# Optimization experiments

Measured on AMD Instinct MI355X. Metric: run time of the kernel, lower is better.

Reference implementation:

```python
import jax, jax.numpy as jnp
import numpy as np

DIM = 1536
NHEADS = 12
HDIM = DIM // NHEADS  # 128
EPS = 1e-6
LOCAL_ATTN_SIZE = 3
SINK_SIZE = 1
MAX_ATTN = 32760 if LOCAL_ATTN_SIZE == -1 else LOCAL_ATTN_SIZE * 1560  # 4680


def _rms(x, g):
    # WanRMSNorm over last dim
    return x * jax.lax.rsqrt(jnp.mean(x * x, axis=-1, keepdims=True) + EPS) * g


def _rope(x, f, h, w, fr, fi, start_frame):
    # x: [b, s, n, d] with s == f*h*w; fr/fi: [1024, d//2] real/imag of complex rotations
    b, s, n, d = x.shape
    c = d // 2
    c0 = c - 2 * (c // 3)
    c1 = c // 3
    fc = jax.lax.complex(fr, fi)  # [1024, c]
    xr = x.reshape(b, s, n, c, 2)
    xc = jax.lax.complex(xr[..., 0], xr[..., 1])  # [b, s, n, c]
    ff = fc[start_frame:start_frame + f, :c0]      # [f, c0]
    fh = fc[:h, c0:c0 + c1]                        # [h, c1]
    fw = fc[:w, c0 + c1:c0 + 2 * c1]               # [w, c1]
    freqs_i = jnp.concatenate([
        jnp.broadcast_to(ff[:, None, None, :], (f, h, w, c0)),
        jnp.broadcast_to(fh[None, :, None, :], (f, h, w, c1)),
        jnp.broadcast_to(fw[None, None, :, :], (f, h, w, c1)),
    ], axis=-1).reshape(1, s, 1, c)
    y = xc * freqs_i
    return jnp.stack([y.real, y.imag], axis=-1).reshape(b, s, n, d)


def _attn(q, k, v):
    # plain SDPA (decode path of the module uses no mask on the gathered window)
    scale = 1.0 / np.sqrt(q.shape[-1]).astype(np.float32)
    logits = jnp.einsum('bqnd,bknd->bnqk', q, k) * scale
    p = jax.nn.softmax(logits, axis=-1)
    return jnp.einsum('bnqk,bknd->bqnd', p, v)


def _forward(x, cache_k, cache_v, freqs_real, freqs_imag,
             wq, bq, wk, bk, wv, bv, wo, bo, gq, gk,
             f_frames, height, width, current_start, global_end_index, local_end_index):
    b, s, _ = x.shape
    n, d = NHEADS, HDIM
    frame_seqlen = height * width
    start_frame = current_start // frame_seqlen

    q = _rms(x @ wq + bq, gq).reshape(b, s, n, d)
    k = _rms(x @ wk + bk, gk).reshape(b, s, n, d)
    v = (x @ wv + bv).reshape(b, s, n, d)

    rq = _rope(q, f_frames, height, width, freqs_real, freqs_imag, start_frame)
    rk = _rope(k, f_frames, height, width, freqs_real, freqs_imag, start_frame)

    current_end = current_start + s
    sink_tokens = SINK_SIZE * frame_seqlen
    kv_size = cache_k.shape[1]
    is_recompute = (current_end <= global_end_index) and (current_start > 0)

    kc, vc = cache_k, cache_v
    if LOCAL_ATTN_SIZE != -1 and current_end > global_end_index and s + local_end_index > kv_size:
        # evict oldest non-sink tokens, roll the rest toward the sink region
        num_evicted = s + local_end_index - kv_size
        num_rolled = local_end_index - num_evicted - sink_tokens
        src = slice(sink_tokens + num_evicted, sink_tokens + num_evicted + num_rolled)
        kc = kc.at[:, sink_tokens:sink_tokens + num_rolled].set(jax.lax.stop_gradient(cache_k[:, src]))
        vc = vc.at[:, sink_tokens:sink_tokens + num_rolled].set(jax.lax.stop_gradient(cache_v[:, src]))
        new_local_end = local_end_index + current_end - global_end_index - num_evicted
    else:
        new_local_end = local_end_index + current_end - global_end_index
    local_start = new_local_end - s
    write_start = max(local_start, sink_tokens) if is_recompute else local_start
    off = max(0, write_start - local_start)
    wl = max(0, new_local_end - write_start)
    if wl > 0:
        kc = kc.at[:, write_start:new_local_end].set(rk[:, off:off + wl])
        vc = vc.at[:, write_start:new_local_end].set(v[:, off:off + wl])

    if sink_tokens > 0:
        budget = MAX_ATTN - sink_tokens
        if budget > 0:
            lo = max(sink_tokens, new_local_end - budget)
            kcat = jnp.concatenate([kc[:, :sink_tokens], kc[:, lo:new_local_end]], axis=1)
            vcat = jnp.concatenate([vc[:, :sink_tokens], vc[:, lo:new_local_end]], axis=1)
        else:
            kcat, vcat = kc[:, :sink_tokens], vc[:, :sink_tokens]
        o = _attn(rq, kcat, vcat)
    else:
        ws = max(0, new_local_end - MAX_ATTN)
        o = _attn(rq, kc[:, ws:new_local_end], vc[:, ws:new_local_end])

    return o.reshape(b, s, DIM) @ wo + bo


def setup_inputs() -> dict:
    key = jax.random.key(0)
    ks = jax.random.split(key, 12)
    B, S, CACHE = 1, 1560, 4680
    sc = 0.02
    # RoPE tables as unit-magnitude complex rotations
    ang = jax.random.uniform(ks[0], (1024, HDIM // 2), jnp.float32, 0.0, 2.0 * np.pi)
    return {
        'x': jax.random.normal(ks[1], (B, S, DIM), jnp.float32),
        'cache_k': jax.random.normal(ks[2], (B, CACHE, NHEADS, HDIM), jnp.float32),
        'cache_v': jax.random.normal(ks[3], (B, CACHE, NHEADS, HDIM), jnp.float32),
        'freqs_real': jnp.cos(ang),
        'freqs_imag': jnp.sin(ang),
        'wq': jax.random.normal(ks[4], (DIM, DIM), jnp.float32) * sc,
        'bq': jnp.zeros((DIM,), jnp.float32),
        'wk': jax.random.normal(ks[5], (DIM, DIM), jnp.float32) * sc,
        'bk': jnp.zeros((DIM,), jnp.float32),
        'wv': jax.random.normal(ks[6], (DIM, DIM), jnp.float32) * sc,
        'bv': jnp.zeros((DIM,), jnp.float32),
        'wo': jax.random.normal(ks[7], (DIM, DIM), jnp.float32) * sc,
        'bo': jnp.zeros((DIM,), jnp.float32),
        'gq': jnp.ones((DIM,), jnp.float32),
        'gk': jnp.ones((DIM,), jnp.float32),
        'f_frames': 1,
        'height': 30,
        'width': 52,
        'current_start': 4680,
        'global_end_index': 4680,
        'local_end_index': 4680,
    }


def reference(x, cache_k, cache_v, freqs_real, freqs_imag,
              wq, bq, wk, bk, wv, bv, wo, bo, gq, gk,
              f_frames, height, width, current_start, global_end_index, local_end_index):
    return _forward(x, cache_k, cache_v, freqs_real, freqs_imag,
                    wq, bq, wk, bk, wv, bv, wo, bo, gq, gk,
                    f_frames, height, width, current_start, global_end_index, local_end_index)
```

## Files before the change

### kernel.cpp

```cpp
#include <hip/hip_runtime.h>
#include <cstdint>
#include <cstddef>

typedef unsigned int  u32;
typedef unsigned short u16;
typedef short s16x8 __attribute__((ext_vector_type(8)));
typedef float f32x4 __attribute__((ext_vector_type(4)));

#define DIM     1536
#define NH      12
#define HD      128
#define SEQ     1560
#define MPAD    1664
#define NKV     4680
#define NKPAD   4736
#define ROLL0   3120
#define NQK     4608
#define START_FRAME 3
#define NEGINF  -3.0e4f
#define NSPLIT  4
#define SPLITKC 1216

__device__ __forceinline__ u16 f2bf(float f){
  u32 u = __builtin_bit_cast(u32, f);
  u32 r = (u + 0x7fffu + ((u >> 16) & 1u)) >> 16;
  return (u16)r;
}

__global__ void k_pre(const float* __restrict__ x, u16* __restrict__ xp,
                      u16* __restrict__ Kc, u16* __restrict__ VT,
                      u16* __restrict__ Qr, u16* __restrict__ Opad,
                      float* __restrict__ sumsq,
                      const float* __restrict__ ck, const float* __restrict__ cv){
  __shared__ u32 tile[64][65];
  int b = blockIdx.x, t = threadIdx.x;
  if (b < 244){
    int i = b * 256 + t;
    uint4 z = make_uint4(0u, 0u, 0u, 0u);
    if (i < 10752){
      int h = i / 896, r = i % 896;
      ((uint4*)(Kc + ((size_t)h * NKPAD + NKV) * 128))[r] = z;
    } else if (i < 21504){
      int j = i - 10752; int row = j / 7, c = j % 7;
      ((uint4*)(VT + (size_t)row * NKPAD + NKV))[c] = z;
    } else if (i < 41472){
      int j = i - 21504; int h = j / 1664, r = j % 1664;
      ((uint4*)(Qr + ((size_t)h * MPAD + SEQ) * 128))[r] = z;
    } else if (i < 61440){
      int r = i - 41472;
      ((uint4*)(Opad + (size_t)SEQ * DIM))[r] = z;
    } else if (i < 62272){
      ((uint4*)sumsq)[i - 61440] = z;
    }
  } else if (b < 1492){
    int i = (b - 244) * 256 + t;
    const int n_src = SEQ * DIM / 8;
    u16 o[8] = {0,0,0,0,0,0,0,0};
    if (i < n_src){
      float4 a = ((const float4*)x)[2*i];
      float4 c = ((const float4*)x)[2*i + 1];
      o[0]=f2bf(a.x); o[1]=f2bf(a.y); o[2]=f2bf(a.z); o[3]=f2bf(a.w);
      o[4]=f2bf(c.x); o[5]=f2bf(c.y); o[6]=f2bf(c.z); o[7]=f2bf(c.w);
    }
    uint4 v = make_uint4((u32)o[0]|((u32)o[1]<<16), (u32)o[2]|((u32)o[3]<<16),
                         (u32)o[4]|((u32)o[5]<<16), (u32)o[6]|((u32)o[7]<<16));
    ((uint4*)xp)[i] = v;
  } else if (b < 3832){
    int i = (b - 1492) * 256 + t;
    int p = i / 192, j = i - p * 192;
    int src = (p < SEQ) ? p : p + SEQ;
    int h = j >> 4, d = (j & 15) * 8;
    const float* s = ck + (size_t)src * DIM + j * 8;
    float4 a = ((const float4*)s)[0], bb = ((const float4*)s)[1];
    uint4 v = make_uint4((u32)f2bf(a.x)|((u32)f2bf(a.y)<<16), (u32)f2bf(a.z)|((u32)f2bf(a.w)<<16),
                         (u32)f2bf(bb.x)|((u32)f2bf(bb.y)<<16), (u32)f2bf(bb.z)|((u32)f2bf(bb.w)<<16));
    *(uint4*)(Kc + (size_t)(h * NKPAD + p) * 128 + d) = v;
  } else {
    int idx = b - 3832;
    int p0 = (idx % 49) * 64, hd0 = (idx / 49) * 64;
    int pr = t >> 4, cg = t & 15;
#pragma unroll
    for (int i = 0; i < 4; i++){
      int p = p0 + pr + i * 16;
      if (p < ROLL0){
        int src = (p < SEQ) ? p : p + SEQ;
        float4 v = *(const float4*)(cv + (size_t)src * DIM + hd0 + cg * 4);
        tile[pr + i*16][cg*4+0] = f2bf(v.x); tile[pr + i*16][cg*4+1] = f2bf(v.y);
        tile[pr + i*16][cg*4+2] = f2bf(v.z); tile[pr + i*16][cg*4+3] = f2bf(v.w);
      }
    }
    __syncthreads();
    int hd = t >> 2, pg = t & 3;
    int pbase = p0 + pg * 16;
    if (pbase < ROLL0){
      u32 wds[8];
#pragma unroll
      for (int j = 0; j < 8; j++)
        wds[j] = (tile[pg*16 + 2*j][hd] & 0xffffu) | (tile[pg*16 + 2*j + 1][hd] << 16);
      u16* q = VT + (size_t)(hd0 + hd) * NKPAD + pbase;
      *(uint4*)q       = make_uint4(wds[0], wds[1], wds[2], wds[3]);
      *(uint4*)(q + 8) = make_uint4(wds[4], wds[5], wds[6], wds[7]);
    }
  }
}

__global__ void k_transpose_w(const float* __restrict__ wq, const float* __restrict__ wk,
                              const float* __restrict__ wv, const float* __restrict__ wo,
                              u16* __restrict__ WTqkv, u16* __restrict__ WTo){
  __shared__ u32 tile[64][65];
  int z = blockIdx.z;
  const float* w = (z==0)?wq:(z==1)?wk:(z==2)?wv:wo;
  u16* dst = (z < 3) ? (WTqkv + (size_t)z * DIM * DIM) : WTo;
  int r0 = blockIdx.x * 64, c0 = blockIdx.y * 64;
  int t = threadIdx.x;
  int rr = t >> 4, cg = t & 15;
#pragma unroll
  for (int i = 0; i < 4; i++){
    int r = rr + i * 16;
    float4 v = *(const float4*)(w + (size_t)(r0 + r) * DIM + c0 + cg * 4);
    tile[r][cg*4+0] = f2bf(v.x); tile[r][cg*4+1] = f2bf(v.y);
    tile[r][cg*4+2] = f2bf(v.z); tile[r][cg*4+3] = f2bf(v.w);
  }
  __syncthreads();
  int c = t >> 2, rg = t & 3;
  u32 wds[8];
#pragma unroll
  for (int j = 0; j < 8; j++)
    wds[j] = (tile[rg*16 + 2*j][c] & 0xffffu) | (tile[rg*16 + 2*j + 1][c] << 16);
  u16* q = dst + (size_t)(c0 + c) * DIM + r0 + rg * 16;
  *(uint4*)q       = make_uint4(wds[0], wds[1], wds[2], wds[3]);
  *(uint4*)(q + 8) = make_uint4(wds[4], wds[5], wds[6], wds[7]);
}

#define LDK 40
__global__ __launch_bounds__(256) void k_gemm_qkv(
    const u16* __restrict__ A, const u16* __restrict__ B,
    const float* __restrict__ biasq, const float* __restrict__ biask, const float* __restrict__ biasv,
    float* __restrict__ Y, float* __restrict__ sumsq, u16* __restrict__ VT){
  __shared__ u16 As[128*LDK];
  __shared__ u16 Bs[128*LDK];
  int m0 = blockIdx.y * 128, n0 = blockIdx.x * 128;
  int t = threadIdx.x, w = t >> 6, lane = t & 63, quad = lane >> 4, lc = lane & 15;
  int wm = w & 1, wn = w >> 1;
  int sr = t >> 1, sh = (t & 1) * 16;
  f32x4 acc[4][4] = {};
  uint4 pa0, pa1, pb0, pb1;
  {
    const uint4* ga = (const uint4*)(A + (size_t)(m0 + sr) * DIM + sh);
    const uint4* gb = (const uint4*)(B + (size_t)(n0 + sr) * DIM + sh);
    pa0 = ga[0]; pa1 = ga[1]; pb0 = gb[0]; pb1 = gb[1];
  }
  for (int kt = 0; kt < DIM/32; kt++){
    __syncthreads();
    *(uint4*)(As + sr * LDK + sh)     = pa0;
    *(uint4*)(As + sr * LDK + sh + 8) = pa1;
    *(uint4*)(Bs + sr * LDK + sh)     = pb0;
    *(uint4*)(Bs + sr * LDK + sh + 8) = pb1;
    __syncthreads();
    if (kt + 1 < DIM/32){
      int k0 = (kt + 1) * 32;
      const uint4* ga = (const uint4*)(A + (size_t)(m0 + sr) * DIM + k0 + sh);
      const uint4* gb = (const uint4*)(B + (size_t)(n0 + sr) * DIM + k0 + sh);
      pa0 = ga[0]; pa1 = ga[1]; pb0 = gb[0]; pb1 = gb[1];
    }
    s16x8 af[4], bf[4];
#pragma unroll
    for (int mt = 0; mt < 4; mt++) af[mt] = *(const s16x8*)(As + (wm*64 + mt*16 + lc) * LDK + quad * 8);
#pragma unroll
    for (int nt = 0; nt < 4; nt++) bf[nt] = *(const s16x8*)(Bs + (wn*64 + nt*16 + lc) * LDK + quad * 8);
#pragma unroll
    for (int mt = 0; mt < 4; mt++)
#pragma unroll
      for (int nt = 0; nt < 4; nt++)
        acc[mt][nt] = __builtin_amdgcn_mfma_f32_16x16x32_bf16(af[mt], bf[nt], acc[mt][nt], 0, 0, 0);
  }
  const float* bias; int cbase; int which;
  if (n0 < DIM)        { bias = biasq; cbase = 0;     which = 0; }
  else if (n0 < 2*DIM) { bias = biask; cbase = DIM;   which = 1; }
  else                 { bias = biasv; cbase = 2*DIM; which = 2; }
  float bvals[4];
#pragma unroll
  for (int nt = 0; nt < 4; nt++) bvals[nt] = bias[n0 - cbase + wn*64 + nt*16 + lc];
  if (which == 2){
#pragma unroll
    for (int mt = 0; mt < 4; mt++){
      int row0 = m0 + wm*64 + mt*16 + quad*4;
      if (row0 < SEQ){
#pragma unroll
        for (int nt = 0; nt < 4; nt++){
          int hd = (n0 - 2*DIM) + wn*64 + nt*16 + lc;
          u32 lo = (u32)f2bf(acc[mt][nt][0] + bvals[nt]) | ((u32)f2bf(acc[mt][nt][1] + bvals[nt]) << 16);
          u32 hi = (u32)f2bf(acc[mt][nt][2] + bvals[nt]) | ((u32)f2bf(acc[mt][nt][3] + bvals[nt]) << 16);
          *(uint2*)(VT + (size_t)hd * NKPAD + ROLL0 + row0) = make_uint2(lo, hi);
        }
      }
    }
  } else {
#pragma unroll
    for (int mt = 0; mt < 4; mt++){
      int row0 = m0 + wm*64 + mt*16 + quad*4;
      float ss[4] = {0.f, 0.f, 0.f, 0.f};
#pragma unroll
      for (int nt = 0; nt < 4; nt++){
        int col = n0 + wn*64 + nt*16 + lc;
#pragma unroll
        for (int r = 0; r < 4; r++){
          float y = acc[mt][nt][r] + bvals[nt];
          Y[(size_t)(row0 + r) * NQK + col] = y;
          ss[r] += y * y;
        }
      }
      float* dst = sumsq + (which ? MPAD : 0);
#pragma unroll
      for (int r = 0; r < 4; r++){
        float v = ss[r];
        v += __shfl_xor(v, 1); v += __shfl_xor(v, 2); v += __shfl_xor(v, 4); v += __shfl_xor(v, 8);
        if (lc == 0) atomicAdd(&dst[row0 + r], v);
      }
    }
  }
}

__global__ void k_rope_qk(const float* __restrict__ Y, const float* __restrict__ sumsq,
                          const float* __restrict__ gq, const float* __restrict__ gk,
                          const float* __restrict__ fre, const float* __restrict__ fim,
                          u16* __restrict__ Qr, u16* __restrict__ Kc){
  int pos = blockIdx.x;
  int t = threadIdx.x;
  float scq = rsqrtf(sumsq[pos]        * (1.0f/1536.0f) + 1e-6f);
  float sck = rsqrtf(sumsq[MPAD + pos] * (1.0f/1536.0f) + 1e-6f);
  int hrow = pos / 52, wrow = pos % 52;
#pragma unroll
  for (int i = 0; i < 3; i++){
    int p = t + i * 256;
    int head = p >> 6, j = p & 63;
    int frow = (j < 22) ? START_FRAME : ((j < 43) ? hrow : wrow);
    float cr = fre[frow * 64 + j], ci = fim[frow * 64 + j];
    int d0 = head * 128 + 2 * j;
    float2 yq = *(const float2*)(Y + (size_t)pos * NQK + d0);
    float qa = yq.x * scq * gq[d0];
    float qb = yq.y * scq * gq[d0 + 1];
    u32 oq = (u32)f2bf(qa * cr - qb * ci) | ((u32)f2bf(qa * ci + qb * cr) << 16);
    *(u32*)(Qr + (size_t)(head * MPAD + pos) * 128 + 2 * j) = oq;
    float2 yk = *(const float2*)(Y + (size_t)pos * NQK + DIM + d0);
    float ka = yk.x * sck * gk[d0];
    float kb = yk.y * sck * gk[d0 + 1];
    u32 ok = (u32)f2bf(ka * cr - kb * ci) | ((u32)f2bf(ka * ci + kb * cr) << 16);
    *(u32*)(Kc + (size_t)(head * NKPAD + ROLL0 + pos) * 128 + 2 * j) = ok;
  }
}

#define DEFER_THR 8.0f
__global__ __launch_bounds__(512, 4) void k_attn(const u16* __restrict__ Qr, const u16* __restrict__ Kc,
                                                 const u16* __restrict__ VT,
                                                 float* __restrict__ Opart, float* __restrict__ ml){
  __shared__ u16 Ks[64 * 128];
  __shared__ u16 Vs[128 * 64];
  int h = blockIdx.y, qb = blockIdx.x, sp = blockIdx.z;
  int t = threadIdx.x, w = t >> 6, lane = t & 63, quad = lane >> 4, lc = lane & 15;
  int qbase = qb * 128 + w * 16;
  const u16* Qbase = Qr + (size_t)(h * MPAD + qbase + lc) * 128;
  s16x8 qf[4];
#pragma unroll
  for (int kk = 0; kk < 4; kk++) qf[kk] = *(const s16x8*)(Qbase + kk * 32 + quad * 8);
  f32x4 oacc[8] = {};
  float m_ = NEGINF;
  float l_ = 0.f;
  const float scale = 0.08838834764831845f;
  const u16* Kh = Kc + (size_t)h * NKPAD * 128;
  const u16* Vh = VT + (size_t)h * 128 * NKPAD;
  int kr0 = t >> 4,          kg0 = (t & 15) * 8;
  int kr1 = (t + 512) >> 4,  kg1 = ((t + 512) & 15) * 8;
  int vd0 = t >> 3,          vp0 = (t & 7) * 8;
  int vd1 = (t + 512) >> 3,  vp1 = ((t + 512) & 7) * 8;
  int ksw0 = kr0 * 128 + (kg0 ^ ((kr0 & 7) << 3));
  int ksw1 = kr1 * 128 + (kg1 ^ ((kr1 & 7) << 3));
  int vsw0 = vd0 * 64  + (vp0 ^ ((vd0 & 7) << 3));
  int vsw1 = vd1 * 64  + (vp1 ^ ((vd1 & 7) << 3));
  int xork = (lc & 7) << 3;
  int aa = (lc + ((quad & 1) << 5)) << 2;
  int ab = aa + 64;
  int hi = quad >> 1;

  int kc0 = sp * SPLITKC;
  int kc1 = (sp == NSPLIT-1) ? NKPAD : kc0 + SPLITKC;
  uint4 kp0, kp1, vq0, vq1;
  {
    int kc = kc0;
    kp0 = *(const uint4*)(Kh + (size_t)(kc + kr0) * 128 + kg0);
    kp1 = *(const uint4*)(Kh + (size_t)(kc + kr1) * 128 + kg1);
    vq0 = *(const uint4*)(Vh + (size_t)vd0 * NKPAD + kc + vp0);
    vq1 = *(const uint4*)(Vh + (size_t)vd1 * NKPAD + kc + vp1);
  }
  for (int kc = kc0; kc < kc1; kc += 64){
    __syncthreads();
    *(uint4*)(Ks + ksw0) = kp0;
    *(uint4*)(Ks + ksw1) = kp1;
    *(uint4*)(Vs + vsw0) = vq0;
    *(uint4*)(Vs + vsw1) = vq1;
    __syncthreads();
    if (kc + 64 < kc1){
      int kn = kc + 64;
      kp0 = *(const uint4*)(Kh + (size_t)(kn + kr0) * 128 + kg0);
      kp1 = *(const uint4*)(Kh + (size_t)(kn + kr1) * 128 + kg1);
      vq0 = *(const uint4*)(Vh + (size_t)vd0 * NKPAD + kn + vp0);
      vq1 = *(const uint4*)(Vh + (size_t)vd1 * NKPAD + kn + vp1);
    }
    float s[4][4];
    __builtin_amdgcn_s_setprio(1);
#pragma unroll
    for (int nt = 0; nt < 4; nt++){
      f32x4 acc = {};
      int p = nt * 16 + lc;
#pragma unroll
      for (int kk = 0; kk < 4; kk++){
        s16x8 kf = *(const s16x8*)(Ks + p * 128 + (((kk * 4 + quad) * 8) ^ xork));
        acc = __builtin_amdgcn_mfma_f32_16x16x32_bf16(kf, qf[kk], acc, 0, 0, 0);
      }
#pragma unroll
      for (int r = 0; r < 4; r++) s[nt][r] = acc[r] * scale;
    }
    __builtin_amdgcn_s_setprio(0);
    if (kc + 64 > NKV){
#pragma unroll
      for (int nt = 0; nt < 4; nt++){
        int keyb = kc + nt * 16 + quad * 4;
#pragma unroll
        for (int r = 0; r < 4; r++) if (keyb + r >= NKV) s[nt][r] = NEGINF;
      }
    }
    float mx = fmaxf(fmaxf(s[0][0], s[0][1]), fmaxf(s[0][2], s[0][3]));
#pragma unroll
    for (int nt = 1; nt < 4; nt++)
      mx = fmaxf(mx, fmaxf(fmaxf(s[nt][0], s[nt][1]), fmaxf(s[nt][2], s[nt][3])));
    mx = fmaxf(mx, __shfl_xor(mx, 16));
    mx = fmaxf(mx, __shfl_xor(mx, 32));
    if (__any(mx > m_ + DEFER_THR)){
      float mnew = fmaxf(m_, mx);
      float alpha = __expf(m_ - mnew);
      m_ = mnew; l_ *= alpha;
      float alr[4];
#pragma unroll
      for (int r = 0; r < 4; r++) alr[r] = __shfl(alpha, quad * 4 + r);
#pragma unroll
      for (int dt = 0; dt < 8; dt++){
        f32x4 oo = oacc[dt];
#pragma unroll
        for (int r = 0; r < 4; r++) oo[r] *= alr[r];
        oacc[dt] = oo;
      }
    }
#pragma unroll
    for (int nt = 0; nt < 4; nt++)
#pragma unroll
      for (int r = 0; r < 4; r++) s[nt][r] = __expf(s[nt][r] - m_);
    float sum = (s[0][0] + s[0][1]) + (s[0][2] + s[0][3]);
#pragma unroll
    for (int nt = 1; nt < 4; nt++)
      sum += (s[nt][0] + s[nt][1]) + (s[nt][2] + s[nt][3]);
    sum += __shfl_xor(sum, 16);
    sum += __shfl_xor(sum, 32);
    l_ += sum;
    u32 w01[4], w23[4];
#pragma unroll
    for (int nt = 0; nt < 4; nt++){
      w01[nt] = (u32)f2bf(s[nt][0]) | ((u32)f2bf(s[nt][1]) << 16);
      w23[nt] = (u32)f2bf(s[nt][2]) | ((u32)f2bf(s[nt][3]) << 16);
    }
    u32 x0, x1;
    uint4 A0, A1;
    x0 = (u32)__builtin_amdgcn_ds_bpermute(aa, (int)w01[0]);
    x1 = (u32)__builtin_amdgcn_ds_bpermute(aa, (int)w01[1]);
    A0.x = hi ? x1 : x0;
    x0 = (u32)__builtin_amdgcn_ds_bpermute(aa, (int)w23[0]);
    x1 = (u32)__builtin_amdgcn_ds_bpermute(aa, (int)w23[1]);
    A0.y = hi ? x1 : x0;
    x0 = (u32)__builtin_amdgcn_ds_bpermute(ab, (int)w01[0]);
    x1 = (u32)__builtin_amdgcn_ds_bpermute(ab, (int)w01[1]);
    A0.z = hi ? x1 : x0;
    x0 = (u32)__builtin_amdgcn_ds_bpermute(ab, (int)w23[0]);
    x1 = (u32)__builtin_amdgcn_ds_bpermute(ab, (int)w23[1]);
    A0.w = hi ? x1 : x0;
    x0 = (u32)__builtin_amdgcn_ds_bpermute(aa, (int)w01[2]);
    x1 = (u32)__builtin_amdgcn_ds_bpermute(aa, (int)w01[3]);
    A1.x = hi ? x1 : x0;
    x0 = (u32)__builtin_amdgcn_ds_bpermute(aa, (int)w23[2]);
    x1 = (u32)__builtin_amdgcn_ds_bpermute(aa, (int)w23[3]);
    A1.y = hi ? x1 : x0;
    x0 = (u32)__builtin_amdgcn_ds_bpermute(ab, (int)w01[2]);
    x1 = (u32)__builtin_amdgcn_ds_bpermute(ab, (int)w01[3]);
    A1.z = hi ? x1 : x0;
    x0 = (u32)__builtin_amdgcn_ds_bpermute(ab, (int)w23[2]);
    x1 = (u32)__builtin_amdgcn_ds_bpermute(ab, (int)w23[3]);
    A1.w = hi ? x1 : x0;
    s16x8 a0 = __builtin_bit_cast(s16x8, A0);
    s16x8 a1 = __builtin_bit_cast(s16x8, A1);
    __builtin_amdgcn_s_setprio(1);
#pragma unroll
    for (int dt = 0; dt < 8; dt++){
      int d = dt * 16 + lc;
      s16x8 v0 = *(const s16x8*)(Vs + d * 64 + ((quad * 8) ^ xork));
      s16x8 v1 = *(const s16x8*)(Vs + d * 64 + ((32 + quad * 8) ^ xork));
      oacc[dt] = __builtin_amdgcn_mfma_f32_16x16x32_bf16(a0, v0, oacc[dt], 0, 0, 0);
      oacc[dt] = __builtin_amdgcn_mfma_f32_16x16x32_bf16(a1, v1, oacc[dt], 0, 0, 0);
    }
    __builtin_amdgcn_s_setprio(0);
  }
  float mr[4], lr[4];
#pragma unroll
  for (int r = 0; r < 4; r++){
    mr[r] = __shfl(m_, quad * 4 + r);
    lr[r] = __shfl(l_, quad * 4 + r);
  }
  float* Ob = Opart + ((size_t)(sp * NH + h) * SEQ) * 128;
  float* mlb = ml + ((size_t)(sp * NH + h) * SEQ) * 2;
#pragma unroll
  for (int dt = 0; dt < 8; dt++)
#pragma unroll
    for (int r = 0; r < 4; r++){
      int row = qbase + quad * 4 + r;
      if (row < SEQ) Ob[(size_t)row * 128 + dt * 16 + lc] = oacc[dt][r];
    }
  if (lc == 0){
#pragma unroll
    for (int r = 0; r < 4; r++){
      int row = qbase + quad * 4 + r;
      if (row < SEQ){
        mlb[row * 2 + 0] = mr[r];
        mlb[row * 2 + 1] = lr[r];
      }
    }
  }
}

__global__ void k_attn_cmb(const float* __restrict__ Opart, const float* __restrict__ ml,
                           u16* __restrict__ Og){
  int row = blockIdx.x, h = blockIdx.y, d = threadIdx.x;
  float m[NSPLIT], l[NSPLIT];
  float M = NEGINF;
#pragma unroll
  for (int s = 0; s < NSPLIT; s++){
    m[s] = ml[((size_t)(s * NH + h) * SEQ + row) * 2 + 0];
    l[s] = ml[((size_t)(s * NH + h) * SEQ + row) * 2 + 1];
    M = fmaxf(M, m[s]);
  }
  float L = 0.f, o = 0.f;
#pragma unroll
  for (int s = 0; s < NSPLIT; s++){
    float wgt = __expf(m[s] - M);
    L += wgt * l[s];
    o += wgt * Opart[((size_t)(s * NH + h) * SEQ + row) * 128 + d];
  }
  Og[(size_t)row * DIM + h * 128 + d] = f2bf(o / L);
}

__global__ __launch_bounds__(256) void k_gemm_out(const u16* __restrict__ A, const u16* __restrict__ B,
                                                  const float* __restrict__ bo, float* __restrict__ out){
  __shared__ u16 As[128*LDK];
  __shared__ u16 Bs[128*LDK];
  int m0 = blockIdx.y * 128, n0 = blockIdx.x * 128;
  int t = threadIdx.x, w = t >> 6, lane = t & 63, quad = lane >> 4, lc = lane & 15;
  int wm = w & 1, wn = w >> 1;
  int sr = t >> 1, sh = (t & 1) * 16;
  f32x4 acc[4][4] = {};
  uint4 pa0, pa1, pb0, pb1;
  {
    const uint4* ga = (const uint4*)(A + (size_t)(m0 + sr) * DIM + sh);
    const uint4* gb = (const uint4*)(B + (size_t)(n0 + sr) * DIM + sh);
    pa0 = ga[0]; pa1 = ga[1]; pb0 = gb[0]; pb1 = gb[1];
  }
  for (int kt = 0; kt < DIM/32; kt++){
    __syncthreads();
    *(uint4*)(As + sr * LDK + sh)     = pa0;
    *(uint4*)(As + sr * LDK + sh + 8) = pa1;
    *(uint4*)(Bs + sr * LDK + sh)     = pb0;
    *(uint4*)(Bs + sr * LDK + sh + 8) = pb1;
    __syncthreads();
    if (kt + 1 < DIM/32){
      int k0 = (kt + 1) * 32;
      const uint4* ga = (const uint4*)(A + (size_t)(m0 + sr) * DIM + k0 + sh);
      const uint4* gb = (const uint4*)(B + (size_t)(n0 + sr) * DIM + k0 + sh);
      pa0 = ga[0]; pa1 = ga[1]; pb0 = gb[0]; pb1 = gb[1];
    }
    s16x8 af[4], bf[4];
#pragma unroll
    for (int mt = 0; mt < 4; mt++) af[mt] = *(const s16x8*)(As + (wm*64 + mt*16 + lc) * LDK + quad * 8);
#pragma unroll
    for (int nt = 0; nt < 4; nt++) bf[nt] = *(const s16x8*)(Bs + (wn*64 + nt*16 + lc) * LDK + quad * 8);
#pragma unroll
    for (int mt = 0; mt < 4; mt++)
#pragma unroll
      for (int nt = 0; nt < 4; nt++)
        acc[mt][nt] = __builtin_amdgcn_mfma_f32_16x16x32_bf16(af[mt], bf[nt], acc[mt][nt], 0, 0, 0);
  }
  float bvals[4];
#pragma unroll
  for (int nt = 0; nt < 4; nt++) bvals[nt] = bo[n0 + wn*64 + nt*16 + lc];
#pragma unroll
  for (int mt = 0; mt < 4; mt++){
    int row0 = m0 + wm*64 + mt*16 + quad*4;
#pragma unroll
    for (int nt = 0; nt < 4; nt++){
      int col = n0 + wn*64 + nt*16 + lc;
#pragma unroll
      for (int r = 0; r < 4; r++){
        int row = row0 + r;
        if (row < SEQ) out[(size_t)row * DIM + col] = acc[mt][nt][r] + bvals[nt];
      }
    }
  }
}

extern "C" void kernel_launch(void* const* d_in, const int* in_sizes, int n_in,
                              void* d_out, int out_size, void* d_ws, size_t ws_size,
                              hipStream_t stream){
  const float* x   = (const float*)d_in[0];
  const float* ck  = (const float*)d_in[1];
  const float* cv  = (const float*)d_in[2];
  const float* fre = (const float*)d_in[3];
  const float* fim = (const float*)d_in[4];
  const float* wq  = (const float*)d_in[5];
  const float* bq  = (const float*)d_in[6];
  const float* wk  = (const float*)d_in[7];
  const float* bk  = (const float*)d_in[8];
  const float* wv  = (const float*)d_in[9];
  const float* bv  = (const float*)d_in[10];
  const float* wo  = (const float*)d_in[11];
  const float* bo  = (const float*)d_in[12];
  const float* gq  = (const float*)d_in[13];
  const float* gk  = (const float*)d_in[14];

  char* ws = (char*)d_ws;
  size_t off = 0;
  u16*   xpad  = (u16*)(ws + off);  off += (size_t)MPAD * DIM * 2;
  u16*   WTqkv = (u16*)(ws + off);  off += (size_t)3 * DIM * DIM * 2;
  float* Y     = (float*)(ws + off); off += (size_t)MPAD * NQK * 4;
  u16*   WTo   = (u16*)(ws + off);  off += (size_t)DIM * DIM * 2;
  float* sumsq = (float*)(ws + off); off += (size_t)2 * MPAD * 4;
  u16*   Qr    = (u16*)(ws + off);  off += (size_t)NH * MPAD * 128 * 2;
  u16*   Kc    = (u16*)(ws + off);  off += (size_t)NH * NKPAD * 128 * 2;
  u16*   VT    = (u16*)(ws + off);  off += (size_t)NH * 128 * NKPAD * 2;
  u16*   Opad  = (u16*)(ws + off);  off += (size_t)MPAD * DIM * 2;
  if (off > ws_size) return;
  float* Opart = (float*)ws;
  float* ml    = (float*)(ws + (size_t)NSPLIT * NH * SEQ * 128 * 4);

  k_pre         <<<dim3(5008), 256, 0, stream>>>(x, xpad, Kc, VT, Qr, Opad, sumsq, ck, cv);
  k_transpose_w <<<dim3(24, 24, 4), 256, 0, stream>>>(wq, wk, wv, wo, WTqkv, WTo);
  k_gemm_qkv    <<<dim3(NQK/128, MPAD/128), 256, 0, stream>>>(xpad, WTqkv, bq, bk, bv, Y, sumsq, VT);
  k_rope_qk     <<<dim3(SEQ), 256, 0, stream>>>(Y, sumsq, gq, gk, fre, fim, Qr, Kc);
  k_attn        <<<dim3(MPAD/128, NH, NSPLIT), 512, 0, stream>>>(Qr, Kc, VT, Opart, ml);
  k_attn_cmb    <<<dim3(SEQ, NH), 128, 0, stream>>>(Opart, ml, Opad);
  k_gemm_out    <<<dim3(DIM/128, MPAD/128), 256, 0, stream>>>(Opad, WTo, bo, (float*)d_out);
}
```

Baseline: 357.4 us.

## Switch attention kernel to 32x32x16 MFMA with 32 query rows per wave

Rewrites the flash-attention inner loop to use 32x32x16 bf16 MFMA tiles, giving each wave 32 query rows instead of 16 and halving the block to 256 threads (4 waves). Each K/V tile loaded into shared memory is now reused by more rows per wave, the shuffle work for the softmax row max/sum shrinks, and the P-matrix lane exchange uses fewer bpermutes. In exchange, register pressure per thread rises (larger accumulators and Q fragments), occupancy hints change, and each thread must issue more global loads per tile.

Result: slower. 495.9 us (+38.8%).

```diff
diff --git a/kernel.cpp b/kernel.cpp
--- a/kernel.cpp
+++ b/kernel.cpp
@@ -6,6 +6,7 @@
 typedef unsigned short u16;
 typedef short s16x8 __attribute__((ext_vector_type(8)));
 typedef float f32x4 __attribute__((ext_vector_type(4)));
+typedef float f32x16 __attribute__((ext_vector_type(16)));
 
 #define DIM     1536
 #define NH      12
@@ -251,184 +252,166 @@
 }
 
 #define DEFER_THR 8.0f
-__global__ __launch_bounds__(512, 4) void k_attn(const u16* __restrict__ Qr, const u16* __restrict__ Kc,
+__global__ __launch_bounds__(256, 2) void k_attn(const u16* __restrict__ Qr, const u16* __restrict__ Kc,
                                                  const u16* __restrict__ VT,
                                                  float* __restrict__ Opart, float* __restrict__ ml){
   __shared__ u16 Ks[64 * 128];
   __shared__ u16 Vs[128 * 64];
   int h = blockIdx.y, qb = blockIdx.x, sp = blockIdx.z;
-  int t = threadIdx.x, w = t >> 6, lane = t & 63, quad = lane >> 4, lc = lane & 15;
-  int qbase = qb * 128 + w * 16;
-  const u16* Qbase = Qr + (size_t)(h * MPAD + qbase + lc) * 128;
-  s16x8 qf[4];
-#pragma unroll
-  for (int kk = 0; kk < 4; kk++) qf[kk] = *(const s16x8*)(Qbase + kk * 32 + quad * 8);
-  f32x4 oacc[8] = {};
-  float m_ = NEGINF;
-  float l_ = 0.f;
+  int t = threadIdx.x, w = t >> 6, lane = t & 63;
+  int l31 = lane & 31, hi = lane >> 5;
+  int qbase = qb * 128 + w * 32;
+  const u16* Qbase = Qr + (size_t)(h * MPAD + qbase + l31) * 128 + hi * 8;
+  s16x8 qf[8];
+#pragma unroll
+  for (int ds = 0; ds < 8; ds++) qf[ds] = *(const s16x8*)(Qbase + ds * 16);
+  f32x16 oacc[4] = {};
+  float m_ = NEGINF, l_ = 0.f;
   const float scale = 0.08838834764831845f;
   const u16* Kh = Kc + (size_t)h * NKPAD * 128;
   const u16* Vh = VT + (size_t)h * 128 * NKPAD;
-  int kr0 = t >> 4,          kg0 = (t & 15) * 8;
-  int kr1 = (t + 512) >> 4,  kg1 = ((t + 512) & 15) * 8;
-  int vd0 = t >> 3,          vp0 = (t & 7) * 8;
-  int vd1 = (t + 512) >> 3,  vp1 = ((t + 512) & 7) * 8;
-  int ksw0 = kr0 * 128 + (kg0 ^ ((kr0 & 7) << 3));
-  int ksw1 = kr1 * 128 + (kg1 ^ ((kr1 & 7) << 3));
-  int vsw0 = vd0 * 64  + (vp0 ^ ((vd0 & 7) << 3));
-  int vsw1 = vd1 * 64  + (vp1 ^ ((vd1 & 7) << 3));
-  int xork = (lc & 7) << 3;
-  int aa = (lc + ((quad & 1) << 5)) << 2;
-  int ab = aa + 64;
-  int hi = quad >> 1;
+  int kr[4], kg[4], ksw[4], vd[4], vp[4], vsw[4];
+#pragma unroll
+  for (int i = 0; i < 4; i++){
+    int n = t + i * 256;
+    kr[i] = n >> 4;  kg[i] = (n & 15) * 8;
+    ksw[i] = kr[i] * 128 + (kg[i] ^ ((kr[i] & 7) << 3));
+    vd[i] = n >> 3;  vp[i] = (n & 7) * 8;
+    vsw[i] = vd[i] * 64 + (vp[i] ^ ((vd[i] & 7) << 3));
+  }
+  int xork = (lane & 7) << 3;
+  int xaddr = (lane ^ 32) << 2;
 
   int kc0 = sp * SPLITKC;
   int kc1 = (sp == NSPLIT-1) ? NKPAD : kc0 + SPLITKC;
-  uint4 kp0, kp1, vq0, vq1;
-  {
-    int kc = kc0;
-    kp0 = *(const uint4*)(Kh + (size_t)(kc + kr0) * 128 + kg0);
-    kp1 = *(const uint4*)(Kh + (size_t)(kc + kr1) * 128 + kg1);
-    vq0 = *(const uint4*)(Vh + (size_t)vd0 * NKPAD + kc + vp0);
-    vq1 = *(const uint4*)(Vh + (size_t)vd1 * NKPAD + kc + vp1);
+  uint4 kp[4], vq[4];
+#pragma unroll
+  for (int i = 0; i < 4; i++){
+    kp[i] = *(const uint4*)(Kh + (size_t)(kc0 + kr[i]) * 128 + kg[i]);
+    vq[i] = *(const uint4*)(Vh + (size_t)vd[i] * NKPAD + kc0 + vp[i]);
   }
   for (int kc = kc0; kc < kc1; kc += 64){
     __syncthreads();
-    *(uint4*)(Ks + ksw0) = kp0;
-    *(uint4*)(Ks + ksw1) = kp1;
-    *(uint4*)(Vs + vsw0) = vq0;
-    *(uint4*)(Vs + vsw1) = vq1;
+#pragma unroll
+    for (int i = 0; i < 4; i++){
+      *(uint4*)(Ks + ksw[i]) = kp[i];
+      *(uint4*)(Vs + vsw[i]) = vq[i];
+    }
     __syncthreads();
     if (kc + 64 < kc1){
       int kn = kc + 64;
-      kp0 = *(const uint4*)(Kh + (size_t)(kn + kr0) * 128 + kg0);
-      kp1 = *(const uint4*)(Kh + (size_t)(kn + kr1) * 128 + kg1);
-      vq0 = *(const uint4*)(Vh + (size_t)vd0 * NKPAD + kn + vp0);
-      vq1 = *(const uint4*)(Vh + (size_t)vd1 * NKPAD + kn + vp1);
-    }
-    float s[4][4];
+#pragma unroll
+      for (int i = 0; i < 4; i++){
+        kp[i] = *(const uint4*)(Kh + (size_t)(kn + kr[i]) * 128 + kg[i]);
+        vq[i] = *(const uint4*)(Vh + (size_t)vd[i] * NKPAD + kn + vp[i]);
+      }
+    }
+    f32x16 sac[2];
     __builtin_amdgcn_s_setprio(1);
 #pragma unroll
-    for (int nt = 0; nt < 4; nt++){
-      f32x4 acc = {};
-      int p = nt * 16 + lc;
-#pragma unroll
-      for (int kk = 0; kk < 4; kk++){
-        s16x8 kf = *(const s16x8*)(Ks + p * 128 + (((kk * 4 + quad) * 8) ^ xork));
-        acc = __builtin_amdgcn_mfma_f32_16x16x32_bf16(kf, qf[kk], acc, 0, 0, 0);
-      }
-#pragma unroll
-      for (int r = 0; r < 4; r++) s[nt][r] = acc[r] * scale;
+    for (int kt = 0; kt < 2; kt++){
+      f32x16 acc = {};
+      const u16* kb = Ks + (kt * 32 + l31) * 128;
+#pragma unroll
+      for (int ds = 0; ds < 8; ds++){
+        s16x8 kf = *(const s16x8*)(kb + (((ds * 2 + hi) * 8) ^ xork));
+        acc = __builtin_amdgcn_mfma_f32_32x32x16_bf16(kf, qf[ds], acc, 0, 0, 0);
+      }
+      sac[kt] = acc;
     }
     __builtin_amdgcn_s_setprio(0);
+#pragma unroll
+    for (int kt = 0; kt < 2; kt++)
+#pragma unroll
+      for (int r = 0; r < 16; r++) sac[kt][r] *= scale;
     if (kc + 64 > NKV){
 #pragma unroll
-      for (int nt = 0; nt < 4; nt++){
-        int keyb = kc + nt * 16 + quad * 4;
-#pragma unroll
-        for (int r = 0; r < 4; r++) if (keyb + r >= NKV) s[nt][r] = NEGINF;
-      }
-    }
-    float mx = fmaxf(fmaxf(s[0][0], s[0][1]), fmaxf(s[0][2], s[0][3]));
-#pragma unroll
-    for (int nt = 1; nt < 4; nt++)
-      mx = fmaxf(mx, fmaxf(fmaxf(s[nt][0], s[nt][1]), fmaxf(s[nt][2], s[nt][3])));
-    mx = fmaxf(mx, __shfl_xor(mx, 16));
+      for (int kt = 0; kt < 2; kt++)
+#pragma unroll
+        for (int r = 0; r < 16; r++){
+          int key = kc + kt * 32 + (r & 3) + 8 * (r >> 2) + 4 * hi;
+          if (key >= NKV) sac[kt][r] = NEGINF;
+        }
+    }
+    float mx = sac[0][0];
+#pragma unroll
+    for (int r = 1; r < 16; r++) mx = fmaxf(mx, sac[0][r]);
+#pragma unroll
+    for (int r = 0; r < 16; r++) mx = fmaxf(mx, sac[1][r]);
     mx = fmaxf(mx, __shfl_xor(mx, 32));
     if (__any(mx > m_ + DEFER_THR)){
       float mnew = fmaxf(m_, mx);
       float alpha = __expf(m_ - mnew);
       m_ = mnew; l_ *= alpha;
-      float alr[4];
-#pragma unroll
-      for (int r = 0; r < 4; r++) alr[r] = __shfl(alpha, quad * 4 + r);
-#pragma unroll
-      for (int dt = 0; dt < 8; dt++){
-        f32x4 oo = oacc[dt];
-#pragma unroll
-        for (int r = 0; r < 4; r++) oo[r] *= alr[r];
-        oacc[dt] = oo;
-      }
-    }
-#pragma unroll
-    for (int nt = 0; nt < 4; nt++)
-#pragma unroll
-      for (int r = 0; r < 4; r++) s[nt][r] = __expf(s[nt][r] - m_);
-    float sum = (s[0][0] + s[0][1]) + (s[0][2] + s[0][3]);
-#pragma unroll
-    for (int nt = 1; nt < 4; nt++)
-      sum += (s[nt][0] + s[nt][1]) + (s[nt][2] + s[nt][3]);
-    sum += __shfl_xor(sum, 16);
+      float ar[16];
+#pragma unroll
+      for (int r = 0; r < 16; r++) ar[r] = __shfl(alpha, (r & 3) + 8 * (r >> 2) + 4 * hi);
+#pragma unroll
+      for (int dt = 0; dt < 4; dt++)
+#pragma unroll
+        for (int r = 0; r < 16; r++) oacc[dt][r] *= ar[r];
+    }
+#pragma unroll
+    for (int kt = 0; kt < 2; kt++)
+#pragma unroll
+      for (int r = 0; r < 16; r++) sac[kt][r] = __expf(sac[kt][r] - m_);
+    float sum = sac[0][0];
+#pragma unroll
+    for (int r = 1; r < 16; r++) sum += sac[0][r];
+#pragma unroll
+    for (int r = 0; r < 16; r++) sum += sac[1][r];
     sum += __shfl_xor(sum, 32);
     l_ += sum;
-    u32 w01[4], w23[4];
-#pragma unroll
-    for (int nt = 0; nt < 4; nt++){
-      w01[nt] = (u32)f2bf(s[nt][0]) | ((u32)f2bf(s[nt][1]) << 16);
-      w23[nt] = (u32)f2bf(s[nt][2]) | ((u32)f2bf(s[nt][3]) << 16);
-    }
-    u32 x0, x1;
-    uint4 A0, A1;
-    x0 = (u32)__builtin_amdgcn_ds_bpermute(aa, (int)w01[0]);
-    x1 = (u32)__builtin_amdgcn_ds_bpermute(aa, (int)w01[1]);
-    A0.x = hi ? x1 : x0;
-    x0 = (u32)__builtin_amdgcn_ds_bpermute(aa, (int)w23[0]);
-    x1 = (u32)__builtin_amdgcn_ds_bpermute(aa, (int)w23[1]);
-    A0.y = hi ? x1 : x0;
-    x0 = (u32)__builtin_amdgcn_ds_bpermute(ab, (int)w01[0]);
-    x1 = (u32)__builtin_amdgcn_ds_bpermute(ab, (int)w01[1]);
-    A0.z = hi ? x1 : x0;
-    x0 = (u32)__builtin_amdgcn_ds_bpermute(ab, (int)w23[0]);
-    x1 = (u32)__builtin_amdgcn_ds_bpermute(ab, (int)w23[1]);
-    A0.w = hi ? x1 : x0;
-    x0 = (u32)__builtin_amdgcn_ds_bpermute(aa, (int)w01[2]);
-    x1 = (u32)__builtin_amdgcn_ds_bpermute(aa, (int)w01[3]);
-    A1.x = hi ? x1 : x0;
-    x0 = (u32)__builtin_amdgcn_ds_bpermute(aa, (int)w23[2]);
-    x1 = (u32)__builtin_amdgcn_ds_bpermute(aa, (int)w23[3]);
-    A1.y = hi ? x1 : x0;
-    x0 = (u32)__builtin_amdgcn_ds_bpermute(ab, (int)w01[2]);
-    x1 = (u32)__builtin_amdgcn_ds_bpermute(ab, (int)w01[3]);
-    A1.z = hi ? x1 : x0;
-    x0 = (u32)__builtin_amdgcn_ds_bpermute(ab, (int)w23[2]);
-    x1 = (u32)__builtin_amdgcn_ds_bpermute(ab, (int)w23[3]);
-    A1.w = hi ? x1 : x0;
-    s16x8 a0 = __builtin_bit_cast(s16x8, A0);
-    s16x8 a1 = __builtin_bit_cast(s16x8, A1);
+    u32 wd[2][4][2];
+#pragma unroll
+    for (int kt = 0; kt < 2; kt++)
+#pragma unroll
+      for (int g = 0; g < 4; g++)
+#pragma unroll
+        for (int hh = 0; hh < 2; hh++)
+          wd[kt][g][hh] = (u32)f2bf(sac[kt][4*g + 2*hh]) | ((u32)f2bf(sac[kt][4*g + 2*hh + 1]) << 16);
+    u32 xp[2][2][2], yp[2][2][2];
+#pragma unroll
+    for (int kt = 0; kt < 2; kt++)
+#pragma unroll
+      for (int j = 0; j < 2; j++)
+#pragma unroll
+        for (int hh = 0; hh < 2; hh++){
+          u32 X = wd[kt][2*j][hh], Yw = wd[kt][2*j + 1][hh];
+          u32 bX = (u32)__builtin_amdgcn_ds_bpermute(xaddr, (int)X);
+          u32 bY = (u32)__builtin_amdgcn_ds_bpermute(xaddr, (int)Yw);
+          xp[kt][j][hh] = hi ? bY : X;
+          yp[kt][j][hh] = hi ? Yw : bX;
+        }
     __builtin_amdgcn_s_setprio(1);
 #pragma unroll
-    for (int dt = 0; dt < 8; dt++){
-      int d = dt * 16 + lc;
-      s16x8 v0 = *(const s16x8*)(Vs + d * 64 + ((quad * 8) ^ xork));
-      s16x8 v1 = *(const s16x8*)(Vs + d * 64 + ((32 + quad * 8) ^ xork));
-      oacc[dt] = __builtin_amdgcn_mfma_f32_16x16x32_bf16(a0, v0, oacc[dt], 0, 0, 0);
-      oacc[dt] = __builtin_amdgcn_mfma_f32_16x16x32_bf16(a1, v1, oacc[dt], 0, 0, 0);
+    for (int ks = 0; ks < 4; ks++){
+      uint4 fa = make_uint4(xp[ks >> 1][ks & 1][0], xp[ks >> 1][ks & 1][1],
+                            yp[ks >> 1][ks & 1][0], yp[ks >> 1][ks & 1][1]);
+      s16x8 a = __builtin_bit_cast(s16x8, fa);
+#pragma unroll
+      for (int dt = 0; dt < 4; dt++){
+        int d = dt * 32 + l31;
+        s16x8 v = *(const s16x8*)(Vs + d * 64 + (((ks * 2 + hi) * 8) ^ xork));
+        oacc[dt] = __builtin_amdgcn_mfma_f32_32x32x16_bf16(a, v, oacc[dt], 0, 0, 0);
+      }
     }
     __builtin_amdgcn_s_setprio(0);
-  }
-  float mr[4], lr[4];
-#pragma unroll
-  for (int r = 0; r < 4; r++){
-    mr[r] = __shfl(m_, quad * 4 + r);
-    lr[r] = __shfl(l_, quad * 4 + r);
   }
   float* Ob = Opart + ((size_t)(sp * NH + h) * SEQ) * 128;
   float* mlb = ml + ((size_t)(sp * NH + h) * SEQ) * 2;
 #pragma unroll
-  for (int dt = 0; dt < 8; dt++)
-#pragma unroll
-    for (int r = 0; r < 4; r++){
-      int row = qbase + quad * 4 + r;
-      if (row < SEQ) Ob[(size_t)row * 128 + dt * 16 + lc] = oacc[dt][r];
-    }
-  if (lc == 0){
-#pragma unroll
-    for (int r = 0; r < 4; r++){
-      int row = qbase + quad * 4 + r;
-      if (row < SEQ){
-        mlb[row * 2 + 0] = mr[r];
-        mlb[row * 2 + 1] = lr[r];
-      }
+  for (int dt = 0; dt < 4; dt++)
+#pragma unroll
+    for (int r = 0; r < 16; r++){
+      int row = qbase + (r & 3) + 8 * (r >> 2) + 4 * hi;
+      if (row < SEQ) Ob[(size_t)row * 128 + dt * 32 + l31] = oacc[dt][r];
+    }
+  if (lane < 32){
+    int row = qbase + lane;
+    if (row < SEQ){
+      mlb[row * 2 + 0] = m_;
+      mlb[row * 2 + 1] = l_;
     }
   }
 }
@@ -549,7 +532,7 @@
   k_transpose_w <<<dim3(24, 24, 4), 256, 0, stream>>>(wq, wk, wv, wo, WTqkv, WTo);
   k_gemm_qkv    <<<dim3(NQK/128, MPAD/128), 256, 0, stream>>>(xpad, WTqkv, bq, bk, bv, Y, sumsq, VT);
   k_rope_qk     <<<dim3(SEQ), 256, 0, stream>>>(Y, sumsq, gq, gk, fre, fim, Qr, Kc);
-  k_attn        <<<dim3(MPAD/128, NH, NSPLIT), 512, 0, stream>>>(Qr, Kc, VT, Opart, ml);
+  k_attn        <<<dim3(MPAD/128, NH, NSPLIT), 256, 0, stream>>>(Qr, Kc, VT, Opart, ml);
   k_attn_cmb    <<<dim3(SEQ, NH), 128, 0, stream>>>(Opart, ml, Opad);
   k_gemm_out    <<<dim3(DIM/128, MPAD/128), 256, 0, stream>>>(Opad, WTo, bo, (float*)d_out);
 }
```

## Merge weight transpose into prep kernel and widen QKV GEMM tile with XCD remap

Applied to the files above, without the earlier changes.

The weight transpose/convert blocks are folded into the k_pre launch as extra blocks, removing one kernel launch. The QKV GEMM moves to 512-thread blocks with 128x256 tiles, so each A tile is reused across twice as many output columns. A block-index remap groups neighbouring tiles onto the same XCD for L2 locality. The epilogue, not shown, must match the new warp-to-tile mapping, and the grid drops to 234 blocks, which may underfill the CUs.

After: 355.8 us. No clear change (-0.4%).

```diff
diff --git a/kernel.cpp b/kernel.cpp
--- a/kernel.cpp
+++ b/kernel.cpp
@@ -31,7 +31,10 @@
                       u16* __restrict__ Kc, u16* __restrict__ VT,
                       u16* __restrict__ Qr, u16* __restrict__ Opad,
                       float* __restrict__ sumsq,
-                      const float* __restrict__ ck, const float* __restrict__ cv){
+                      const float* __restrict__ ck, const float* __restrict__ cv,
+                      const float* __restrict__ wq, const float* __restrict__ wk,
+                      const float* __restrict__ wv, const float* __restrict__ wo,
+                      u16* __restrict__ WTqkv, u16* __restrict__ WTo){
   __shared__ u32 tile[64][65];
   int b = blockIdx.x, t = threadIdx.x;
   if (b < 244){
@@ -75,7 +78,7 @@
     uint4 v = make_uint4((u32)f2bf(a.x)|((u32)f2bf(a.y)<<16), (u32)f2bf(a.z)|((u32)f2bf(a.w)<<16),
                          (u32)f2bf(bb.x)|((u32)f2bf(bb.y)<<16), (u32)f2bf(bb.z)|((u32)f2bf(bb.w)<<16));
     *(uint4*)(Kc + (size_t)(h * NKPAD + p) * 128 + d) = v;
-  } else {
+  } else if (b < 5008){
     int idx = b - 3832;
     int p0 = (idx % 49) * 64, hd0 = (idx / 49) * 64;
     int pr = t >> 4, cg = t & 15;
@@ -101,67 +104,66 @@
       *(uint4*)q       = make_uint4(wds[0], wds[1], wds[2], wds[3]);
       *(uint4*)(q + 8) = make_uint4(wds[4], wds[5], wds[6], wds[7]);
     }
-  }
-}
-
-__global__ void k_transpose_w(const float* __restrict__ wq, const float* __restrict__ wk,
-                              const float* __restrict__ wv, const float* __restrict__ wo,
-                              u16* __restrict__ WTqkv, u16* __restrict__ WTo){
-  __shared__ u32 tile[64][65];
-  int z = blockIdx.z;
-  const float* w = (z==0)?wq:(z==1)?wk:(z==2)?wv:wo;
-  u16* dst = (z < 3) ? (WTqkv + (size_t)z * DIM * DIM) : WTo;
-  int r0 = blockIdx.x * 64, c0 = blockIdx.y * 64;
-  int t = threadIdx.x;
-  int rr = t >> 4, cg = t & 15;
-#pragma unroll
-  for (int i = 0; i < 4; i++){
-    int r = rr + i * 16;
-    float4 v = *(const float4*)(w + (size_t)(r0 + r) * DIM + c0 + cg * 4);
-    tile[r][cg*4+0] = f2bf(v.x); tile[r][cg*4+1] = f2bf(v.y);
-    tile[r][cg*4+2] = f2bf(v.z); tile[r][cg*4+3] = f2bf(v.w);
-  }
-  __syncthreads();
-  int c = t >> 2, rg = t & 3;
-  u32 wds[8];
-#pragma unroll
-  for (int j = 0; j < 8; j++)
-    wds[j] = (tile[rg*16 + 2*j][c] & 0xffffu) | (tile[rg*16 + 2*j + 1][c] << 16);
-  u16* q = dst + (size_t)(c0 + c) * DIM + r0 + rg * 16;
-  *(uint4*)q       = make_uint4(wds[0], wds[1], wds[2], wds[3]);
-  *(uint4*)(q + 8) = make_uint4(wds[4], wds[5], wds[6], wds[7]);
+  } else {
+    int idx = b - 5008;
+    int z = idx / 576, rem = idx % 576;
+    const float* w = (z==0)?wq:(z==1)?wk:(z==2)?wv:wo;
+    u16* dst = (z < 3) ? (WTqkv + (size_t)z * DIM * DIM) : WTo;
+    int r0 = (rem % 24) * 64, c0 = (rem / 24) * 64;
+    int rr = t >> 4, cg = t & 15;
+#pragma unroll
+    for (int i = 0; i < 4; i++){
+      int r = rr + i * 16;
+      float4 v = *(const float4*)(w + (size_t)(r0 + r) * DIM + c0 + cg * 4);
+      tile[r][cg*4+0] = f2bf(v.x); tile[r][cg*4+1] = f2bf(v.y);
+      tile[r][cg*4+2] = f2bf(v.z); tile[r][cg*4+3] = f2bf(v.w);
+    }
+    __syncthreads();
+    int c = t >> 2, rg = t & 3;
+    u32 wds[8];
+#pragma unroll
+    for (int j = 0; j < 8; j++)
+      wds[j] = (tile[rg*16 + 2*j][c] & 0xffffu) | (tile[rg*16 + 2*j + 1][c] << 16);
+    u16* q = dst + (size_t)(c0 + c) * DIM + r0 + rg * 16;
+    *(uint4*)q       = make_uint4(wds[0], wds[1], wds[2], wds[3]);
+    *(uint4*)(q + 8) = make_uint4(wds[4], wds[5], wds[6], wds[7]);
+  }
 }
 
 #define LDK 40
-__global__ __launch_bounds__(256) void k_gemm_qkv(
+__global__ __launch_bounds__(512) void k_gemm_qkv(
     const u16* __restrict__ A, const u16* __restrict__ B,
     const float* __restrict__ biasq, const float* __restrict__ biask, const float* __restrict__ biasv,
     float* __restrict__ Y, float* __restrict__ sumsq, u16* __restrict__ VT){
   __shared__ u16 As[128*LDK];
-  __shared__ u16 Bs[128*LDK];
-  int m0 = blockIdx.y * 128, n0 = blockIdx.x * 128;
+  __shared__ u16 Bs[256*LDK];
+  int orig = blockIdx.y * 18 + blockIdx.x;
+  int xcd = orig & 7, jj = orig >> 3;
+  int wg = (xcd < 2 ? xcd * 30 : 60 + (xcd - 2) * 29) + jj;
+  int n0 = (wg % 18) * 256;
+  int m0 = (wg / 18) * 128;
   int t = threadIdx.x, w = t >> 6, lane = t & 63, quad = lane >> 4, lc = lane & 15;
   int wm = w & 1, wn = w >> 1;
-  int sr = t >> 1, sh = (t & 1) * 16;
+  int ar = t >> 2, ac = (t & 3) * 8;
+  int br = t >> 1, bc = (t & 1) * 16;
   f32x4 acc[4][4] = {};
-  uint4 pa0, pa1, pb0, pb1;
+  uint4 pa, pb0, pb1;
   {
-    const uint4* ga = (const uint4*)(A + (size_t)(m0 + sr) * DIM + sh);
-    const uint4* gb = (const uint4*)(B + (size_t)(n0 + sr) * DIM + sh);
-    pa0 = ga[0]; pa1 = ga[1]; pb0 = gb[0]; pb1 = gb[1];
+    pa = *(const uint4*)(A + (size_t)(m0 + ar) * DIM + ac);
+    const uint4* gb = (const uint4*)(B + (size_t)(n0 + br) * DIM + bc);
+    pb0 = gb[0]; pb1 = gb[1];
   }
   for (int kt = 0; kt < DIM/32; kt++){
     __syncthreads();
-    *(uint4*)(As + sr * LDK + sh)     = pa0;
-    *(uint4*)(As + sr * LDK + sh + 8) = pa1;
-    *(uint4*)(Bs + sr * LDK + sh)     = pb0;
-    *(uint4*)(Bs + sr * LDK + sh + 8) = pb1;
+    *(uint4*)(As + ar * LDK + ac)     = pa;
+    *(uint4*)(Bs + br * LDK + bc)     = pb0;
+    *(uint4*)(Bs + br * LDK + bc + 8) = pb1;
     __syncthreads();
     if (kt + 1 < DIM/32){
       int k0 = (kt + 1) * 32;
-      const uint4* ga = (const uint4*)(A + (size_t)(m0 + sr) * DIM + k0 + sh);
-      const uint4* gb = (const uint4*)(B + (size_t)(n0 + sr) * DIM + k0 + sh);
-      pa0 = ga[0]; pa1 = ga[1]; pb0 = gb[0]; pb1 = gb[1];
+      pa = *(const uint4*)(A + (size_t)(m0 + ar) * DIM + k0 + ac);
+      const uint4* gb = (const uint4*)(B + (size_t)(n0 + br) * DIM + k0 + bc);
+      pb0 = gb[0]; pb1 = gb[1];
     }
     s16x8 af[4], bf[4];
 #pragma unroll
@@ -545,9 +547,9 @@
   float* Opart = (float*)ws;
   float* ml    = (float*)(ws + (size_t)NSPLIT * NH * SEQ * 128 * 4);
 
-  k_pre         <<<dim3(5008), 256, 0, stream>>>(x, xpad, Kc, VT, Qr, Opad, sumsq, ck, cv);
-  k_transpose_w <<<dim3(24, 24, 4), 256, 0, stream>>>(wq, wk, wv, wo, WTqkv, WTo);
-  k_gemm_qkv    <<<dim3(NQK/128, MPAD/128), 256, 0, stream>>>(xpad, WTqkv, bq, bk, bv, Y, sumsq, VT);
+  k_pre         <<<dim3(7312), 256, 0, stream>>>(x, xpad, Kc, VT, Qr, Opad, sumsq, ck, cv,
+                                                 wq, wk, wv, wo, WTqkv, WTo);
+  k_gemm_qkv    <<<dim3(18, 13), 512, 0, stream>>>(xpad, WTqkv, bq, bk, bv, Y, sumsq, VT);
   k_rope_qk     <<<dim3(SEQ), 256, 0, stream>>>(Y, sumsq, gq, gk, fre, fim, Qr, Kc);
   k_attn        <<<dim3(MPAD/128, NH, NSPLIT), 512, 0, stream>>>(Qr, Kc, VT, Opart, ml);
   k_attn_cmb    <<<dim3(SEQ, NH), 128, 0, stream>>>(Opart, ml, Opad);
```
